# Optimization experiments

Measured on AMD Instinct MI355X. Metric: run time of the kernel, lower is better.

## Reference

```python
import jax, jax.numpy as jnp
import numpy as np

N_QUBITS = 12
RANK = 1024
K = 4            # outcomes per qubit
D = 2 ** N_QUBITS
N_IDX = 1_000_000


def setup_inputs() -> dict:
    key = jax.random.key(0)
    k1, k2, k3, k4 = jax.random.split(key, 4)
    params = jax.random.normal(k1, (2, D, RANK), dtype=jnp.float32)
    M_real = jax.random.normal(k2, (K, 2, 2), dtype=jnp.float32)
    M_imag = jax.random.normal(k3, (K, 2, 2), dtype=jnp.float32)
    P_idxs = jax.random.randint(k4, (N_IDX,), 0, K ** N_QUBITS, dtype=jnp.int64)
    return {"params": params, "M_real": M_real, "M_imag": M_imag, "P_idxs": P_idxs}


def _qmt(rho, M, n_qubits):
    """Born rule: P[s1..sN] = Tr[(M_{s1} x ... x M_{sN}) rho].
    Sequential per-qubit contraction; T has shape [K^n, 2^(N-n), 2^(N-n)]."""
    T = rho[None, :, :]  # axes: (done outcomes, row legs j, col legs i)
    for _ in range(n_qubits):
        k, r, c = T.shape[0], T.shape[1] // 2, T.shape[2] // 2
        Tt = T.reshape(k, 2, r, 2, c)  # (k, j_n, j_rest, i_n, i_rest)
        # Tr contribution: sum_{i,j} M[s,i,j] * rho[j,i]
        T = jnp.einsum('sij,kjait->ksat', M, Tt).reshape(k * M.shape[0], r, c)
    return T.reshape(-1)  # [K^N] complex


def reference(params, M_real, M_imag, P_idxs):
    # rho = U U^H / Tr(U U^H)
    U = jax.lax.complex(params[0], params[1])            # [D, RANK] complex64
    rho = U @ U.conj().T                                  # [D, D]
    rho = rho / jnp.trace(rho)
    M = jax.lax.complex(M_real, M_imag)                   # [K, 2, 2] complex64
    P_all = _qmt(rho, M, N_QUBITS).real                   # [K^N] float32
    return P_all[P_idxs]
```

## Files before the change

kernel.cpp:

```cpp
#include <hip/hip_runtime.h>

#define D 4096
#define RANK 1024
#define UELEMS 4194304ULL
#define NTOT 16777216ULL
#define QSCALE 16000.0f

typedef __attribute__((ext_vector_type(4))) int i32x4;

__device__ float g_inv_tr[1];
__device__ float g_scale[D];
__device__ float g_mdre[16];
__device__ float g_mdim[16];

static __device__ __forceinline__ void load_lds16(const void* g, void* l) {
    __builtin_amdgcn_global_load_lds(
        (const __attribute__((address_space(1))) unsigned int*)g,
        (__attribute__((address_space(3))) unsigned int*)l, 16, 0, 0);
}

#define MFMA_I8 __builtin_amdgcn_mfma_i32_16x16x64_i8

__global__ __launch_bounds__(256) void convert_w_i8(const float* __restrict__ P,
                                                    const float* __restrict__ Mre,
                                                    const float* __restrict__ Mim,
                                                    char* __restrict__ Wh,
                                                    char* __restrict__ Wl)
{
    if (blockIdx.x == 0 && threadIdx.x < 16) {
        const int s = threadIdx.x >> 2, i = (threadIdx.x >> 1) & 1, j = threadIdx.x & 1;
        g_mdre[threadIdx.x] =  Mre[s * 4 + j * 2 + i];
        g_mdim[threadIdx.x] = -Mim[s * 4 + j * 2 + i];
    }

    const int w = threadIdx.x >> 6, lane = threadIdx.x & 63;
    const int row = blockIdx.x * 4 + w;

    float ur[16], ui[16];
    const float* pr = P + (size_t)row * RANK + lane * 16;
    const float* pi = P + UELEMS + (size_t)row * RANK + lane * 16;
    #pragma unroll
    for (int q = 0; q < 4; ++q) {
        const float4 a = ((const float4*)pr)[q];
        const float4 b = ((const float4*)pi)[q];
        ur[q * 4 + 0] = a.x; ur[q * 4 + 1] = a.y; ur[q * 4 + 2] = a.z; ur[q * 4 + 3] = a.w;
        ui[q * 4 + 0] = b.x; ui[q * 4 + 1] = b.y; ui[q * 4 + 2] = b.z; ui[q * 4 + 3] = b.w;
    }
    float mx = 0.f;
    #pragma unroll
    for (int e = 0; e < 16; ++e)
        mx = fmaxf(mx, fmaxf(fabsf(ur[e]), fabsf(ui[e])));
    #pragma unroll
    for (int off = 1; off < 64; off <<= 1)
        mx = fmaxf(mx, __shfl_xor(mx, off));
    const float inv = mx > 0.f ? QSCALE / mx : 0.f;
    if (lane == 0) g_scale[row] = mx / QSCALE;

    int hr[16], lr[16], hi[16], li[16];
    #pragma unroll
    for (int e = 0; e < 16; ++e) {
        float q = ur[e] * inv;
        float hf = rintf(q * 0.0078125f);
        hr[e] = (int)hf; lr[e] = (int)rintf(q - 128.f * hf);
        q = ui[e] * inv;
        hf = rintf(q * 0.0078125f);
        hi[e] = (int)hf; li[e] = (int)rintf(q - 128.f * hf);
    }
    uint4 phr, plr, phi, pli;
    unsigned* dst[4] = {(unsigned*)&phr, (unsigned*)&plr, (unsigned*)&phi, (unsigned*)&pli};
    #pragma unroll
    for (int q = 0; q < 4; ++q) {
        unsigned a = 0, b = 0, c = 0, d = 0;
        #pragma unroll
        for (int k = 0; k < 4; ++k) {
            const int sh = k * 8;
            a |= (unsigned)(hr[q * 4 + k] & 255) << sh;
            b |= (unsigned)(lr[q * 4 + k] & 255) << sh;
            c |= (unsigned)(hi[q * 4 + k] & 255) << sh;
            d |= (unsigned)(li[q * 4 + k] & 255) << sh;
        }
        dst[0][q] = a; dst[1][q] = b; dst[2][q] = c; dst[3][q] = d;
    }
    const size_t b1 = (size_t)row * 2048 + lane * 16;
    *(uint4*)&Wh[b1] = phr;          *(uint4*)&Wl[b1] = plr;
    *(uint4*)&Wh[b1 + 1024] = phi;   *(uint4*)&Wl[b1 + 1024] = pli;
}

__global__ __launch_bounds__(512, 2) void gemm_rho_i8(const char* __restrict__ Wh,
                                                      const char* __restrict__ Wl,
                                                      float2* __restrict__ rho)
{
    __shared__ __align__(16) char sA[2][4][128 * 64];
    __shared__ __align__(16) char sB[2][4][64 * 64];

    const int g = blockIdx.x;
    int bi = (int)((sqrtf(4.f * (float)g + 1.f) - 1.f) * 0.5f);
    while (bi > 0 && bi * (bi + 1) > g) --bi;
    while ((bi + 1) * (bi + 2) <= g) ++bi;
    const int bj = g - bi * (bi + 1);
    const int row0 = bi << 7, col0 = bj << 6;

    const int t = threadIdx.x;
    const int lane = t & 63, w = t >> 6;
    const int wr = w >> 1, wc = w & 1;

    const int ra = t >> 2;
    const int kca = (t & 3) ^ ((ra >> 1) & 3);
    const size_t aoff = (size_t)(row0 + ra) * 2048 + kca * 16;
    const int ldsAo = t * 16;
    const int tb = t & 255;
    const int rb = tb >> 2;
    const int kcb = (t & 3) ^ ((rb >> 1) & 3);
    const int hiw = (t >= 256) ? 1 : 0;
    const size_t boff = (size_t)(col0 + rb) * 2048 + kcb * 16 + hiw * 1024;
    const int ldsB0o = hiw * 8192 + tb * 16;
    const int ldsB1o = ldsB0o + 4096;

    const int m = lane & 15, gq = lane >> 4;
    const int fko = (gq ^ ((m >> 1) & 3)) * 16;

    i32x4 rehh[2][2], remx[2][2], iphh[2][2], ipmx[2][2], iqhh[2][2], iqmx[2][2];
    #pragma unroll
    for (int i = 0; i < 2; ++i)
        #pragma unroll
        for (int j = 0; j < 2; ++j) {
            rehh[i][j] = (i32x4){0, 0, 0, 0}; remx[i][j] = (i32x4){0, 0, 0, 0};
            iphh[i][j] = (i32x4){0, 0, 0, 0}; ipmx[i][j] = (i32x4){0, 0, 0, 0};
            iqhh[i][j] = (i32x4){0, 0, 0, 0}; iqmx[i][j] = (i32x4){0, 0, 0, 0};
        }

    char* const sA0 = &sA[0][0][0];
    char* const sB0 = &sB[0][0][0];

    load_lds16(Wh + aoff,        sA0 + ldsAo);
    load_lds16(Wl + aoff,        sA0 + 8192  + ldsAo);
    load_lds16(Wh + aoff + 1024, sA0 + 16384 + ldsAo);
    load_lds16(Wl + aoff + 1024, sA0 + 24576 + ldsAo);
    load_lds16(Wh + boff,        sB0 + ldsB0o);
    load_lds16(Wl + boff,        sB0 + ldsB1o);
    __syncthreads();

#define DO_MFMA_J(j)                                                          \
    _Pragma("unroll")                                                         \
    for (int i = 0; i < 2; ++i) {                                             \
        i32x4 r;                                                              \
        r = rehh[i][j];                                                       \
        r = MFMA_I8(fa1h[i], b1h, r, 0, 0, 0);                                \
        r = MFMA_I8(fa2h[i], b2h, r, 0, 0, 0);                                \
        rehh[i][j] = r;                                                       \
        r = remx[i][j];                                                       \
        r = MFMA_I8(fa1h[i], b1l, r, 0, 0, 0);                                \
        r = MFMA_I8(fa1l[i], b1h, r, 0, 0, 0);                                \
        r = MFMA_I8(fa2h[i], b2l, r, 0, 0, 0);                                \
        r = MFMA_I8(fa2l[i], b2h, r, 0, 0, 0);                                \
        remx[i][j] = r;                                                       \
        r = MFMA_I8(fa2h[i], b1h, iphh[i][j], 0, 0, 0); iphh[i][j] = r;       \
        r = ipmx[i][j];                                                       \
        r = MFMA_I8(fa2h[i], b1l, r, 0, 0, 0);                                \
        r = MFMA_I8(fa2l[i], b1h, r, 0, 0, 0);                                \
        ipmx[i][j] = r;                                                       \
        r = MFMA_I8(fa1h[i], b2h, iqhh[i][j], 0, 0, 0); iqhh[i][j] = r;       \
        r = iqmx[i][j];                                                       \
        r = MFMA_I8(fa1h[i], b2l, r, 0, 0, 0);                                \
        r = MFMA_I8(fa1l[i], b2h, r, 0, 0, 0);                                \
        iqmx[i][j] = r;                                                       \
    }

    #pragma unroll 2
    for (int kt = 0; kt < 16; ++kt) {
        const int cur = kt & 1;
        const char* sAc = sA0 + cur * 32768;
        const char* sBc = sB0 + cur * 16384;
        char* sAn = sA0 + (cur ^ 1) * 32768;
        char* sBn = sB0 + (cur ^ 1) * 16384;
        const size_t ko = (size_t)(kt + 1) * 64;

        i32x4 fa1h[2], fa1l[2], fa2h[2], fa2l[2];
        i32x4 b1h, b1l, b2h, b2l;

        #pragma unroll
        for (int i = 0; i < 2; ++i) {
            const int off = (wr * 32 + i * 16 + m) * 64 + fko;
            fa1h[i] = *(const i32x4*)(sAc + off);
            fa1l[i] = *(const i32x4*)(sAc + 8192  + off);
            fa2h[i] = *(const i32x4*)(sAc + 16384 + off);
            fa2l[i] = *(const i32x4*)(sAc + 24576 + off);
        }
        {
            const int off = (wc * 32 + m) * 64 + fko;
            b1h = *(const i32x4*)(sBc + off);
            b1l = *(const i32x4*)(sBc + 4096  + off);
            b2h = *(const i32x4*)(sBc + 8192  + off);
            b2l = *(const i32x4*)(sBc + 12288 + off);
        }
        if (kt < 15) {
            load_lds16(Wh + aoff + ko,        sAn + ldsAo);
            load_lds16(Wl + aoff + ko,        sAn + 8192  + ldsAo);
            load_lds16(Wh + aoff + ko + 1024, sAn + 16384 + ldsAo);
            load_lds16(Wl + aoff + ko + 1024, sAn + 24576 + ldsAo);
        }
        __builtin_amdgcn_s_barrier();
        asm volatile("s_waitcnt lgkmcnt(0)" ::: "memory");
        __builtin_amdgcn_sched_barrier(0);
        __builtin_amdgcn_s_setprio(1);
        DO_MFMA_J(0)
        __builtin_amdgcn_s_setprio(0);
        __builtin_amdgcn_s_barrier();

        {
            const int off = (wc * 32 + 16 + m) * 64 + fko;
            b1h = *(const i32x4*)(sBc + off);
            b1l = *(const i32x4*)(sBc + 4096  + off);
            b2h = *(const i32x4*)(sBc + 8192  + off);
            b2l = *(const i32x4*)(sBc + 12288 + off);
        }
        if (kt < 15) {
            load_lds16(Wh + boff + ko, sBn + ldsB0o);
            load_lds16(Wl + boff + ko, sBn + ldsB1o);
        }
        __builtin_amdgcn_s_barrier();
        asm volatile("s_waitcnt lgkmcnt(0)" ::: "memory");
        __builtin_amdgcn_sched_barrier(0);
        __builtin_amdgcn_s_setprio(1);
        DO_MFMA_J(1)
        __builtin_amdgcn_s_setprio(0);

        __syncthreads();
    }
#undef DO_MFMA_J

    #pragma unroll
    for (int j = 0; j < 2; ++j) {
        const int col = col0 + wc * 32 + j * 16 + m;
        const float sc = g_scale[col];
        const int c64 = col >> 6;
        #pragma unroll
        for (int i = 0; i < 2; ++i) {
            #pragma unroll
            for (int r = 0; r < 4; ++r) {
                const int row = row0 + wr * 32 + i * 16 + gq * 4 + r;
                const float s2 = g_scale[row] * sc;
                const float re = s2 * (16384.f * (float)rehh[i][j][r] + 128.f * (float)remx[i][j][r]);
                const float im = s2 * (16384.f * (float)(iphh[i][j][r] - iqhh[i][j][r])
                                      + 128.f * (float)(ipmx[i][j][r] - iqmx[i][j][r]));
                const int r64 = row >> 6;
                if (r64 > c64 || row >= col) rho[(size_t)row * D + col] = make_float2(re, im);
                if (r64 == c64 && row > col) rho[(size_t)col * D + row] = make_float2(re, -im);
            }
        }
    }
}

__global__ void trace_inv(const float2* __restrict__ rho)
{
    __shared__ float red[256];
    float s = 0.f;
    for (int d = threadIdx.x; d < D; d += 256)
        s += rho[(size_t)d * (D + 1)].x;
    red[threadIdx.x] = s;
    __syncthreads();
    for (int off = 128; off > 0; off >>= 1) {
        if (threadIdx.x < off) red[threadIdx.x] += red[threadIdx.x + off];
        __syncthreads();
    }
    if (threadIdx.x == 0) g_inv_tr[0] = 1.0f / red[0];
}

static __device__ __forceinline__ void qmt2(float2* x,
                                            const float* __restrict__ Mre,
                                            const float* __restrict__ Mim)
{
    float2 y[16];
    #pragma unroll
    for (int sb = 0; sb < 4; ++sb)
        #pragma unroll
        for (int ja = 0; ja < 2; ++ja)
            #pragma unroll
            for (int ia = 0; ia < 2; ++ia) {
                float2 acc = make_float2(0.f, 0.f);
                #pragma unroll
                for (int ib = 0; ib < 2; ++ib)
                    #pragma unroll
                    for (int jb = 0; jb < 2; ++jb) {
                        const float mr = Mre[sb * 4 + ib * 2 + jb];
                        const float mi = Mim[sb * 4 + ib * 2 + jb];
                        const float2 v = x[(ja * 2 + jb) * 4 + ia * 2 + ib];
                        acc.x += mr * v.x - mi * v.y;
                        acc.y += mr * v.y + mi * v.x;
                    }
                y[sb * 4 + ja * 2 + ia] = acc;
            }
    #pragma unroll
    for (int sa = 0; sa < 4; ++sa)
        #pragma unroll
        for (int sb = 0; sb < 4; ++sb) {
            float2 acc = make_float2(0.f, 0.f);
            #pragma unroll
            for (int ia = 0; ia < 2; ++ia)
                #pragma unroll
                for (int ja = 0; ja < 2; ++ja) {
                    const float mr = Mre[sa * 4 + ia * 2 + ja];
                    const float mi = Mim[sa * 4 + ia * 2 + ja];
                    const float2 v = y[sb * 4 + ja * 2 + ia];
                    acc.x += mr * v.x - mi * v.y;
                    acc.y += mr * v.y + mi * v.x;
                }
            x[sa * 4 + sb] = acc;
        }
}

static __device__ __forceinline__ void pA_pipeline(float2* x, float2* X, const int t,
                                                   const float* __restrict__ mre,
                                                   const float* __restrict__ mim)
{
    qmt2(x, mre, mim);
    #pragma unroll
    for (int d = 0; d < 16; ++d) X[t * 17 + d] = x[d];
    __syncthreads();
    const int a2 = t >> 6, t2 = (t >> 4) & 3, d1 = t & 15;
    #pragma unroll
    for (int j2 = 0; j2 < 4; ++j2)
        #pragma unroll
        for (int i2 = 0; i2 < 4; ++i2)
            x[j2 * 4 + i2] = X[((a2 * 4 + j2) * 16 + t2 * 4 + i2) * 17 + d1];
    __syncthreads();
    qmt2(x, mre, mim);
    #pragma unroll
    for (int d = 0; d < 16; ++d) X[(a2 * 4 + t2) * 257 + d * 16 + d1] = x[d];
    __syncthreads();
    const int e2 = t >> 4, e1 = t & 15;
    #pragma unroll
    for (int j2 = 0; j2 < 4; ++j2)
        #pragma unroll
        for (int i2 = 0; i2 < 4; ++i2)
            x[j2 * 4 + i2] = X[(j2 * 4 + i2) * 257 + e2 * 16 + e1];
    qmt2(x, mre, mim);
}

__global__ __launch_bounds__(256) void qmt_pAh(const float2* __restrict__ in,
                                               float2* __restrict__ out,
                                               const float* __restrict__ Mre,
                                               const float* __restrict__ Mim)
{
    __shared__ __align__(16) float2 X[256 * 17];
    const int t = threadIdx.x;
    const int g = blockIdx.x;
    int rr = (int)((sqrtf(8.f * (float)g + 1.f) - 1.f) * 0.5f);
    while (rr * (rr + 1) / 2 > g) --rr;
    while ((rr + 1) * (rr + 2) / 2 <= g) ++rr;
    const int cc = g - rr * (rr + 1) / 2;

    const int a4 = t >> 4, t4 = t & 15;
    float2 x0[16], x[16];
    #pragma unroll
    for (int j2 = 0; j2 < 4; ++j2) {
        const float2* p = in + ((size_t)(rr * 64 + a4 * 4 + j2)) * 4096 + cc * 64 + t4 * 4;
        const float4 v0 = ((const float4*)p)[0];
        const float4 v1 = ((const float4*)p)[1];
        x0[j2 * 4 + 0] = make_float2(v0.x, v0.y);
        x0[j2 * 4 + 1] = make_float2(v0.z, v0.w);
        x0[j2 * 4 + 2] = make_float2(v1.x, v1.y);
        x0[j2 * 4 + 3] = make_float2(v1.z, v1.w);
    }

    #pragma unroll
    for (int q = 0; q < 16; ++q) x[q] = x0[q];
    pA_pipeline(x, X, t, Mre, Mim);
    const int e2 = t >> 4, e1 = t & 15;
    const size_t ob0 = (size_t)(rr * 64 + cc) * 4096 + e2 * 16 + e1;
    #pragma unroll
    for (int d = 0; d < 16; ++d) out[ob0 + (size_t)d * 256] = x[d];

    if (rr != cc) {
        __syncthreads();
        #pragma unroll
        for (int q = 0; q < 16; ++q) x[q] = x0[q];
        pA_pipeline(x, X, t, g_mdre, g_mdim);
        const size_t ob1 = (size_t)(cc * 64 + rr) * 4096 + e2 * 16 + e1;
        #pragma unroll
        for (int d = 0; d < 16; ++d)
            out[ob1 + (size_t)d * 256] = make_float2(x[d].x, -x[d].y);
    }
}

static __device__ __forceinline__ void qmt_stage_cb_half(float2* x,
                                                         const float* __restrict__ Mre,
                                                         const float* __restrict__ Mim)
{
    #pragma unroll
    for (int jb = 0; jb < 2; ++jb) {
        float2 y[16];
        #pragma unroll
        for (int sc = 0; sc < 4; ++sc)
            #pragma unroll
            for (int ii = 0; ii < 4; ++ii) {
                float2 acc = make_float2(0.f, 0.f);
                #pragma unroll
                for (int ic = 0; ic < 2; ++ic)
                    #pragma unroll
                    for (int jc = 0; jc < 2; ++jc) {
                        const float mr = Mre[sc * 4 + ic * 2 + jc];
                        const float mi = Mim[sc * 4 + ic * 2 + jc];
                        const float2 v = x[jb * 16 + jc * 8 + ii * 2 + ic];
                        acc.x += mr * v.x - mi * v.y;
                        acc.y += mr * v.y + mi * v.x;
                    }
                y[sc * 4 + ii] = acc;
            }
        #pragma unroll
        for (int q = 0; q < 16; ++q) x[jb * 16 + q] = y[q];
    }
    #pragma unroll
    for (int sc = 0; sc < 4; ++sc) {
        float2 z[8];
        #pragma unroll
        for (int sb = 0; sb < 4; ++sb)
            #pragma unroll
            for (int ia = 0; ia < 2; ++ia) {
                float2 acc = make_float2(0.f, 0.f);
                #pragma unroll
                for (int ib = 0; ib < 2; ++ib)
                    #pragma unroll
                    for (int jb = 0; jb < 2; ++jb) {
                        const float mr = Mre[sb * 4 + ib * 2 + jb];
                        const float mi = Mim[sb * 4 + ib * 2 + jb];
                        const float2 v = x[jb * 16 + sc * 4 + ia * 2 + ib];
                        acc.x += mr * v.x - mi * v.y;
                        acc.y += mr * v.y + mi * v.x;
                    }
                z[sb * 2 + ia] = acc;
            }
        #pragma unroll
        for (int sb = 0; sb < 4; ++sb)
            #pragma unroll
            for (int ia = 0; ia < 2; ++ia)
                x[(sb >> 1) * 16 + sc * 4 + ia * 2 + (sb & 1)] = z[sb * 2 + ia];
    }
}

#define STAGE_A_COEFFS                                                        \
    float Are[2][2], Aim[2][2], Bre[2][2], Bim[2][2];                         \
    _Pragma("unroll")                                                         \
    for (int sal = 0; sal < 2; ++sal)                                         \
        _Pragma("unroll")                                                     \
        for (int ia = 0; ia < 2; ++ia) {                                      \
            const int sa = 2 * h + sal;                                       \
            Are[sal][ia] = Mre[sa * 4 + ia * 2 + h];                          \
            Aim[sal][ia] = Mim[sa * 4 + ia * 2 + h];                          \
            Bre[sal][ia] = Mre[sa * 4 + ia * 2 + (1 - h)];                    \
            Bim[sal][ia] = Mim[sa * 4 + ia * 2 + (1 - h)];                    \
        }

__global__ __launch_bounds__(256) void qmt_p3(const float2* __restrict__ in,
                                              float2* __restrict__ out,
                                              const float* __restrict__ Mre,
                                              const float* __restrict__ Mim)
{
    const int t = threadIdx.x;
    const int h = (t >> 5) & 1;
    const int idx = blockIdx.x * 4 + (t >> 6);
    const int rc = idx >> 7;
    const int r3 = rc >> 3, c3 = rc & 7;
    const int s = (idx & 127) * 32 + (t & 31);

    float2 x[32];
    #pragma unroll
    for (int jb = 0; jb < 2; ++jb)
        #pragma unroll
        for (int jc = 0; jc < 2; ++jc) {
            const int j3 = 4 * h + 2 * jb + jc;
            #pragma unroll
            for (int i3 = 0; i3 < 8; ++i3)
                x[jb * 16 + jc * 8 + i3] =
                    in[(size_t)((r3 * 8 + j3) * 64 + c3 * 8 + i3) * 4096 + s];
        }

    qmt_stage_cb_half(x, Mre, Mim);

    STAGE_A_COEFFS
    const size_t ob = ((size_t)(r3 * 8 + c3) * 64) * 4096 + s;
    #pragma unroll
    for (int sbH = 0; sbH < 2; ++sbH)
        #pragma unroll
        for (int sc = 0; sc < 4; ++sc)
            #pragma unroll
            for (int sbL = 0; sbL < 2; ++sbL) {
                const int q = sbH * 16 + sc * 4 + sbL;
                const float2 o0 = x[q], o1 = x[q + 2];
                float2 r0, r1;
                r0.x = __shfl_xor(o0.x, 32); r0.y = __shfl_xor(o0.y, 32);
                r1.x = __shfl_xor(o1.x, 32); r1.y = __shfl_xor(o1.y, 32);
                const int sb = sbH * 2 + sbL;
                #pragma unroll
                for (int sal = 0; sal < 2; ++sal) {
                    const float re = Are[sal][0] * o0.x - Aim[sal][0] * o0.y
                                   + Are[sal][1] * o1.x - Aim[sal][1] * o1.y
                                   + Bre[sal][0] * r0.x - Bim[sal][0] * r0.y
                                   + Bre[sal][1] * r1.x - Bim[sal][1] * r1.y;
                    const float im = Are[sal][0] * o0.y + Aim[sal][0] * o0.x
                                   + Are[sal][1] * o1.y + Aim[sal][1] * o1.x
                                   + Bre[sal][0] * r0.y + Bim[sal][0] * r0.x
                                   + Bre[sal][1] * r1.y + Bim[sal][1] * r1.x;
                    const int s3 = (2 * h + sal) * 16 + sb * 4 + sc;
                    out[ob + (size_t)s3 * 4096] = make_float2(re, im);
                }
            }
}

__global__ __launch_bounds__(256) void qmt_p4(const float2* __restrict__ in,
                                              float* __restrict__ out,
                                              const float* __restrict__ Mre,
                                              const float* __restrict__ Mim)
{
    const int t = threadIdx.x;
    const int h = (t >> 5) & 1;
    const int s = (blockIdx.x * 4 + (t >> 6)) * 32 + (t & 31);

    float2 x[32];
    #pragma unroll
    for (int jb = 0; jb < 2; ++jb)
        #pragma unroll
        for (int jc = 0; jc < 2; ++jc) {
            const int j3 = 4 * h + 2 * jb + jc;
            #pragma unroll
            for (int i3 = 0; i3 < 8; ++i3)
                x[jb * 16 + jc * 8 + i3] = in[(size_t)(j3 * 8 + i3) * 262144 + s];
        }

    qmt_stage_cb_half(x, Mre, Mim);

    STAGE_A_COEFFS
    const size_t ob = (size_t)(s >> 5) * 2048 + (s & 31);
    #pragma unroll
    for (int sbH = 0; sbH < 2; ++sbH)
        #pragma unroll
        for (int sc = 0; sc < 4; ++sc)
            #pragma unroll
            for (int sbL = 0; sbL < 2; ++sbL) {
                const int q = sbH * 16 + sc * 4 + sbL;
                const float2 o0 = x[q], o1 = x[q + 2];
                float2 r0, r1;
                r0.x = __shfl_xor(o0.x, 32); r0.y = __shfl_xor(o0.y, 32);
                r1.x = __shfl_xor(o1.x, 32); r1.y = __shfl_xor(o1.y, 32);
                const int sb = sbH * 2 + sbL;
                #pragma unroll
                for (int sal = 0; sal < 2; ++sal) {
                    const float re = Are[sal][0] * o0.x - Aim[sal][0] * o0.y
                                   + Are[sal][1] * o1.x - Aim[sal][1] * o1.y
                                   + Bre[sal][0] * r0.x - Bim[sal][0] * r0.y
                                   + Bre[sal][1] * r1.x - Bim[sal][1] * r1.y;
                    const int s3 = (2 * h + sal) * 16 + sb * 4 + sc;
                    out[ob + (size_t)s3 * 32] = re;
                }
            }
}

__global__ void gather_idx(const float* __restrict__ P, const int* __restrict__ idxs,
                           float* __restrict__ out, const int n)
{
    const int i = blockIdx.x * 256 + threadIdx.x;
    if (i < n) {
        const int idx = idxs[i];
        const int s = idx & 262143;
        const size_t pos = (size_t)(s >> 5) * 2048 + (size_t)(idx >> 18) * 32 + (s & 31);
        out[i] = P[pos] * g_inv_tr[0];
    }
}

extern "C" void kernel_launch(void* const* d_in, const int* in_sizes, int n_in,
                              void* d_out, int out_size, void* d_ws, size_t ws_size,
                              hipStream_t stream)
{
    const float* params = (const float*)d_in[0];
    const float* Mre    = (const float*)d_in[1];
    const float* Mim    = (const float*)d_in[2];
    const int*   idxs   = (const int*)d_in[3];
    float*       out    = (float*)d_out;

    float* ws = (float*)d_ws;
    float2* A  = (float2*)ws;
    float2* Bp = (float2*)(ws + 2 * NTOT);
    char* Wh = (char*)Bp;
    char* Wl = Wh + (size_t)D * 2048;

    convert_w_i8<<<1024, 256, 0, stream>>>(params, Mre, Mim, Wh, Wl);
    gemm_rho_i8<<<1056, 512, 0, stream>>>(Wh, Wl, A);
    trace_inv<<<1, 256, 0, stream>>>(A);

    qmt_pAh<<<2080, 256, 0, stream>>>(A, Bp, Mre, Mim);
    qmt_p3<<<2048, 256, 0, stream>>>(Bp, A, Mre, Mim);
    qmt_p4<<<2048, 256, 0, stream>>>(A, (float*)Bp, Mre, Mim);

    gather_idx<<<(out_size + 255) / 256, 256, 0, stream>>>((float*)Bp, idxs, out, out_size);
}
```

Measured before the change: 395.9 us.

## Shrink rho GEMM tiles to 64x64 with 256 threads and simplify pipeline

The int8 split-precision Gram GEMM moves from 128x64 triangular tiles with 512 threads to 64x64 tiles with 256 threads, doubling the grid to 2080 blocks over the lower triangle. The k-loop now issues all next-tile LDS loads up front and reads both B fragments at once. This drops the intra-iteration barriers and split B staging. Smaller tiles give more blocks and a simpler schedule, but halve A/B reuse per block, increasing global and LDS traffic.

```diff
diff --git a/kernel.cpp b/kernel.cpp
--- a/kernel.cpp
+++ b/kernel.cpp
@@ -86,19 +86,19 @@
     *(uint4*)&Wh[b1 + 1024] = phi;   *(uint4*)&Wl[b1 + 1024] = pli;
 }
 
-__global__ __launch_bounds__(512, 2) void gemm_rho_i8(const char* __restrict__ Wh,
+__global__ __launch_bounds__(256, 2) void gemm_rho_i8(const char* __restrict__ Wh,
                                                       const char* __restrict__ Wl,
                                                       float2* __restrict__ rho)
 {
-    __shared__ __align__(16) char sA[2][4][128 * 64];
+    __shared__ __align__(16) char sA[2][4][64 * 64];
     __shared__ __align__(16) char sB[2][4][64 * 64];
 
     const int g = blockIdx.x;
-    int bi = (int)((sqrtf(4.f * (float)g + 1.f) - 1.f) * 0.5f);
-    while (bi > 0 && bi * (bi + 1) > g) --bi;
-    while ((bi + 1) * (bi + 2) <= g) ++bi;
-    const int bj = g - bi * (bi + 1);
-    const int row0 = bi << 7, col0 = bj << 6;
+    int bi = (int)((sqrtf(8.f * (float)g + 1.f) - 1.f) * 0.5f);
+    while (bi * (bi + 1) / 2 > g) --bi;
+    while ((bi + 1) * (bi + 2) / 2 <= g) ++bi;
+    const int bj = g - bi * (bi + 1) / 2;
+    const int row0 = bi << 6, col0 = bj << 6;
 
     const int t = threadIdx.x;
     const int lane = t & 63, w = t >> 6;
@@ -107,14 +107,8 @@
     const int ra = t >> 2;
     const int kca = (t & 3) ^ ((ra >> 1) & 3);
     const size_t aoff = (size_t)(row0 + ra) * 2048 + kca * 16;
-    const int ldsAo = t * 16;
-    const int tb = t & 255;
-    const int rb = tb >> 2;
-    const int kcb = (t & 3) ^ ((rb >> 1) & 3);
-    const int hiw = (t >= 256) ? 1 : 0;
-    const size_t boff = (size_t)(col0 + rb) * 2048 + kcb * 16 + hiw * 1024;
-    const int ldsB0o = hiw * 8192 + tb * 16;
-    const int ldsB1o = ldsB0o + 4096;
+    const size_t boff = (size_t)(col0 + ra) * 2048 + kca * 16;
+    const int ldso = t * 16;
 
     const int m = lane & 15, gq = lane >> 4;
     const int fko = (gq ^ ((m >> 1) & 3)) * 16;
@@ -132,12 +126,14 @@
     char* const sA0 = &sA[0][0][0];
     char* const sB0 = &sB[0][0][0];
 
-    load_lds16(Wh + aoff,        sA0 + ldsAo);
-    load_lds16(Wl + aoff,        sA0 + 8192  + ldsAo);
-    load_lds16(Wh + aoff + 1024, sA0 + 16384 + ldsAo);
-    load_lds16(Wl + aoff + 1024, sA0 + 24576 + ldsAo);
-    load_lds16(Wh + boff,        sB0 + ldsB0o);
-    load_lds16(Wl + boff,        sB0 + ldsB1o);
+    load_lds16(Wh + aoff,        sA0 + ldso);
+    load_lds16(Wl + aoff,        sA0 + 4096  + ldso);
+    load_lds16(Wh + aoff + 1024, sA0 + 8192  + ldso);
+    load_lds16(Wl + aoff + 1024, sA0 + 12288 + ldso);
+    load_lds16(Wh + boff,        sB0 + ldso);
+    load_lds16(Wl + boff,        sB0 + 4096  + ldso);
+    load_lds16(Wh + boff + 1024, sB0 + 8192  + ldso);
+    load_lds16(Wl + boff + 1024, sB0 + 12288 + ldso);
     __syncthreads();
 
 #define DO_MFMA_J(j)                                                          \
@@ -145,83 +141,68 @@
     for (int i = 0; i < 2; ++i) {                                             \
         i32x4 r;                                                              \
         r = rehh[i][j];                                                       \
-        r = MFMA_I8(fa1h[i], b1h, r, 0, 0, 0);                                \
-        r = MFMA_I8(fa2h[i], b2h, r, 0, 0, 0);                                \
+        r = MFMA_I8(fa1h[i], b1h[j], r, 0, 0, 0);                             \
+        r = MFMA_I8(fa2h[i], b2h[j], r, 0, 0, 0);                             \
         rehh[i][j] = r;                                                       \
         r = remx[i][j];                                                       \
-        r = MFMA_I8(fa1h[i], b1l, r, 0, 0, 0);                                \
-        r = MFMA_I8(fa1l[i], b1h, r, 0, 0, 0);                                \
-        r = MFMA_I8(fa2h[i], b2l, r, 0, 0, 0);                                \
-        r = MFMA_I8(fa2l[i], b2h, r, 0, 0, 0);                                \
+        r = MFMA_I8(fa1h[i], b1l[j], r, 0, 0, 0);                             \
+        r = MFMA_I8(fa1l[i], b1h[j], r, 0, 0, 0);                             \
+        r = MFMA_I8(fa2h[i], b2l[j], r, 0, 0, 0);                             \
+        r = MFMA_I8(fa2l[i], b2h[j], r, 0, 0, 0);                             \
         remx[i][j] = r;                                                       \
-        r = MFMA_I8(fa2h[i], b1h, iphh[i][j], 0, 0, 0); iphh[i][j] = r;       \
+        r = MFMA_I8(fa2h[i], b1h[j], iphh[i][j], 0, 0, 0); iphh[i][j] = r;    \
         r = ipmx[i][j];                                                       \
-        r = MFMA_I8(fa2h[i], b1l, r, 0, 0, 0);                                \
-        r = MFMA_I8(fa2l[i], b1h, r, 0, 0, 0);                                \
+        r = MFMA_I8(fa2h[i], b1l[j], r, 0, 0, 0);                             \
+        r = MFMA_I8(fa2l[i], b1h[j], r, 0, 0, 0);                             \
         ipmx[i][j] = r;                                                       \
-        r = MFMA_I8(fa1h[i], b2h, iqhh[i][j], 0, 0, 0); iqhh[i][j] = r;       \
+        r = MFMA_I8(fa1h[i], b2h[j], iqhh[i][j], 0, 0, 0); iqhh[i][j] = r;    \
         r = iqmx[i][j];                                                       \
-        r = MFMA_I8(fa1h[i], b2l, r, 0, 0, 0);                                \
-        r = MFMA_I8(fa1l[i], b2h, r, 0, 0, 0);                                \
+        r = MFMA_I8(fa1h[i], b2l[j], r, 0, 0, 0);                             \
+        r = MFMA_I8(fa1l[i], b2h[j], r, 0, 0, 0);                             \
         iqmx[i][j] = r;                                                       \
     }
 
     #pragma unroll 2
     for (int kt = 0; kt < 16; ++kt) {
         const int cur = kt & 1;
-        const char* sAc = sA0 + cur * 32768;
+        const char* sAc = sA0 + cur * 16384;
         const char* sBc = sB0 + cur * 16384;
-        char* sAn = sA0 + (cur ^ 1) * 32768;
+        char* sAn = sA0 + (cur ^ 1) * 16384;
         char* sBn = sB0 + (cur ^ 1) * 16384;
         const size_t ko = (size_t)(kt + 1) * 64;
 
+        if (kt < 15) {
+            load_lds16(Wh + aoff + ko,        sAn + ldso);
+            load_lds16(Wl + aoff + ko,        sAn + 4096  + ldso);
+            load_lds16(Wh + aoff + ko + 1024, sAn + 8192  + ldso);
+            load_lds16(Wl + aoff + ko + 1024, sAn + 12288 + ldso);
+            load_lds16(Wh + boff + ko,        sBn + ldso);
+            load_lds16(Wl + boff + ko,        sBn + 4096  + ldso);
+            load_lds16(Wh + boff + ko + 1024, sBn + 8192  + ldso);
+            load_lds16(Wl + boff + ko + 1024, sBn + 12288 + ldso);
+        }
+
         i32x4 fa1h[2], fa1l[2], fa2h[2], fa2l[2];
-        i32x4 b1h, b1l, b2h, b2l;
-
+        i32x4 b1h[2], b1l[2], b2h[2], b2l[2];
         #pragma unroll
         for (int i = 0; i < 2; ++i) {
             const int off = (wr * 32 + i * 16 + m) * 64 + fko;
             fa1h[i] = *(const i32x4*)(sAc + off);
-            fa1l[i] = *(const i32x4*)(sAc + 8192  + off);
-            fa2h[i] = *(const i32x4*)(sAc + 16384 + off);
-            fa2l[i] = *(const i32x4*)(sAc + 24576 + off);
-        }
-        {
-            const int off = (wc * 32 + m) * 64 + fko;
-            b1h = *(const i32x4*)(sBc + off);
-            b1l = *(const i32x4*)(sBc + 4096  + off);
-            b2h = *(const i32x4*)(sBc + 8192  + off);
-            b2l = *(const i32x4*)(sBc + 12288 + off);
-        }
-        if (kt < 15) {
-            load_lds16(Wh + aoff + ko,        sAn + ldsAo);
-            load_lds16(Wl + aoff + ko,        sAn + 8192  + ldsAo);
-            load_lds16(Wh + aoff + ko + 1024, sAn + 16384 + ldsAo);
-            load_lds16(Wl + aoff + ko + 1024, sAn + 24576 + ldsAo);
-        }
-        __builtin_amdgcn_s_barrier();
-        asm volatile("s_waitcnt lgkmcnt(0)" ::: "memory");
-        __builtin_amdgcn_sched_barrier(0);
+            fa1l[i] = *(const i32x4*)(sAc + 4096  + off);
+            fa2h[i] = *(const i32x4*)(sAc + 8192  + off);
+            fa2l[i] = *(const i32x4*)(sAc + 12288 + off);
+        }
+        #pragma unroll
+        for (int j = 0; j < 2; ++j) {
+            const int off = (wc * 32 + j * 16 + m) * 64 + fko;
+            b1h[j] = *(const i32x4*)(sBc + off);
+            b1l[j] = *(const i32x4*)(sBc + 4096  + off);
+            b2h[j] = *(const i32x4*)(sBc + 8192  + off);
+            b2l[j] = *(const i32x4*)(sBc + 12288 + off);
+        }
+
         __builtin_amdgcn_s_setprio(1);
         DO_MFMA_J(0)
-        __builtin_amdgcn_s_setprio(0);
-        __builtin_amdgcn_s_barrier();
-
-        {
-            const int off = (wc * 32 + 16 + m) * 64 + fko;
-            b1h = *(const i32x4*)(sBc + off);
-            b1l = *(const i32x4*)(sBc + 4096  + off);
-            b2h = *(const i32x4*)(sBc + 8192  + off);
-            b2l = *(const i32x4*)(sBc + 12288 + off);
-        }
-        if (kt < 15) {
-            load_lds16(Wh + boff + ko, sBn + ldsB0o);
-            load_lds16(Wl + boff + ko, sBn + ldsB1o);
-        }
-        __builtin_amdgcn_s_barrier();
-        asm volatile("s_waitcnt lgkmcnt(0)" ::: "memory");
-        __builtin_amdgcn_sched_barrier(0);
-        __builtin_amdgcn_s_setprio(1);
         DO_MFMA_J(1)
         __builtin_amdgcn_s_setprio(0);
 
@@ -584,7 +565,7 @@
     char* Wl = Wh + (size_t)D * 2048;
 
     convert_w_i8<<<1024, 256, 0, stream>>>(params, Mre, Mim, Wh, Wl);
-    gemm_rho_i8<<<1056, 512, 0, stream>>>(Wh, Wl, A);
+    gemm_rho_i8<<<2080, 256, 0, stream>>>(Wh, Wl, A);
     trace_inv<<<1, 256, 0, stream>>>(A);
 
     qmt_pAh<<<2080, 256, 0, stream>>>(A, Bp, Mre, Mim);
```

Measured after the change: 388.5 us. Within noise of the previous version (-1.9%).
